# Kernel optimization log

Hardware: AMD Instinct MI355X
Metric: run time of the kernel (lower is better)

Reference implementation:

```python
import jax, jax.numpy as jnp
import numpy as np


def setup_inputs() -> dict:
    key = jax.random.key(0)
    k1, k2 = jax.random.split(key)
    N = 50000
    E = 800000
    out_features = 64
    edge = jax.random.randint(k1, (2, E), 0, N, dtype=jnp.int64)
    edge_w = jax.random.normal(k2, (E, out_features), dtype=jnp.float32)
    return {"edge": edge, "edge_w": edge_w, "N": N, "E": E, "out_features": out_features}


def reference(edge, edge_w, N, E, out_features):
    # sparse_coo_tensor(edge, edge_w, [N, N, F]) summed over dim=1 reduces to a
    # segment-sum of edge values over the row (source) index edge[0].
    # output[i, f] = sum_{e: edge[0,e]==i} edge_w[e, f]   -> [N, out_features]
    return jax.ops.segment_sum(edge_w, edge[0], num_segments=N)
```

## Files before the change

kernel.cpp:

```cpp
#include <hip/hip_runtime.h>


#define TILE 1024

__global__ __launch_bounds__(256) void hist_kernel(
    const int* __restrict__ edge0, int* __restrict__ counts, int E)
{
    int t = blockIdx.x * blockDim.x + threadIdx.x;
    int base = t * 4;
    if (base + 3 < E) {
        int4 r = ((const int4*)edge0)[t];
        atomicAdd(&counts[r.x], 1);
        atomicAdd(&counts[r.y], 1);
        atomicAdd(&counts[r.z], 1);
        atomicAdd(&counts[r.w], 1);
    } else {
        for (int i = base; i < E; ++i) atomicAdd(&counts[edge0[i]], 1);
    }
}

__global__ __launch_bounds__(256) void scan_partial(
    const int* __restrict__ counts, int* __restrict__ tileSum, int N)
{
    __shared__ int wsum[4];
    int t = threadIdx.x;
    int base = blockIdx.x * TILE + t * 4;
    int s = 0;
    #pragma unroll
    for (int k = 0; k < 4; ++k) {
        int i = base + k;
        if (i < N) s += counts[i];
    }
    for (int off = 1; off < 64; off <<= 1) s += __shfl_xor(s, off);
    if ((t & 63) == 0) wsum[t >> 6] = s;
    __syncthreads();
    if (t == 0) tileSum[blockIdx.x] = wsum[0] + wsum[1] + wsum[2] + wsum[3];
}

__global__ __launch_bounds__(64) void scan_tiles(
    const int* __restrict__ tileSum, int* __restrict__ tileOff, int numTiles,
    int* __restrict__ offsets, int N, int E)
{
    int t = threadIdx.x;
    int v0 = (t < numTiles) ? tileSum[t] : 0;
    int v = v0;
    for (int off = 1; off < 64; off <<= 1) {
        int u = __shfl_up(v, off);
        if (t >= off) v += u;
    }
    if (t < numTiles) tileOff[t] = v - v0;
    if (t == 0) offsets[N] = E;
}

__global__ __launch_bounds__(256) void scan_final(
    const int* __restrict__ counts, const int* __restrict__ tileOff,
    int* __restrict__ offsets, int N)
{
    __shared__ int wtot[4];
    int t = threadIdx.x;
    int lane = t & 63, wv = t >> 6;
    int base = blockIdx.x * TILE + t * 4;
    int c[4]; int s = 0;
    #pragma unroll
    for (int k = 0; k < 4; ++k) {
        int i = base + k;
        c[k] = (i < N) ? counts[i] : 0;
        s += c[k];
    }
    int inc = s;
    for (int off = 1; off < 64; off <<= 1) {
        int u = __shfl_up(inc, off);
        if (lane >= off) inc += u;
    }
    if (lane == 63) wtot[wv] = inc;
    __syncthreads();
    int wpre = 0;
    for (int w = 0; w < wv; ++w) wpre += wtot[w];
    int pre = tileOff[blockIdx.x] + wpre + (inc - s);
    #pragma unroll
    for (int k = 0; k < 4; ++k) {
        int i = base + k;
        if (i < N) offsets[i] = pre;
        pre += c[k];
    }
}

__global__ __launch_bounds__(256) void scatter_kernel(
    const int* __restrict__ edge0, int* __restrict__ cursor,
    int* __restrict__ ids, int E)
{
    int t = blockIdx.x * blockDim.x + threadIdx.x;
    int base = t * 4;
    if (base + 3 < E) {
        int4 r = ((const int4*)edge0)[t];
        ids[atomicAdd(&cursor[r.x], 1)] = base;
        ids[atomicAdd(&cursor[r.y], 1)] = base + 1;
        ids[atomicAdd(&cursor[r.z], 1)] = base + 2;
        ids[atomicAdd(&cursor[r.w], 1)] = base + 3;
    } else {
        for (int i = base; i < E; ++i) ids[atomicAdd(&cursor[edge0[i]], 1)] = i;
    }
}

__global__ __launch_bounds__(256) void reduce_kernel(
    const int* __restrict__ offsets, const int* __restrict__ ids,
    const float4* __restrict__ w4, float4* __restrict__ out4, int N)
{
    int row = blockIdx.x * 4 + (threadIdx.x >> 6);
    if (row >= N) return;
    int lane = threadIdx.x & 63;
    int sub = lane >> 3, g = lane & 7;
    int beg = offsets[row], end = offsets[row + 1];
    float4 a0 = make_float4(0.f, 0.f, 0.f, 0.f);
    float4 a1 = make_float4(0.f, 0.f, 0.f, 0.f);
    int j = beg + sub;
    for (; j + 8 < end; j += 16) {
        int e0 = ids[j], e1 = ids[j + 8];
        float4 w00 = w4[(size_t)e0 * 16 + g * 2];
        float4 w01 = w4[(size_t)e0 * 16 + g * 2 + 1];
        float4 w10 = w4[(size_t)e1 * 16 + g * 2];
        float4 w11 = w4[(size_t)e1 * 16 + g * 2 + 1];
        a0.x += w00.x + w10.x; a0.y += w00.y + w10.y;
        a0.z += w00.z + w10.z; a0.w += w00.w + w10.w;
        a1.x += w01.x + w11.x; a1.y += w01.y + w11.y;
        a1.z += w01.z + w11.z; a1.w += w01.w + w11.w;
    }
    if (j < end) {
        int e = ids[j];
        float4 w0 = w4[(size_t)e * 16 + g * 2];
        float4 w1 = w4[(size_t)e * 16 + g * 2 + 1];
        a0.x += w0.x; a0.y += w0.y; a0.z += w0.z; a0.w += w0.w;
        a1.x += w1.x; a1.y += w1.y; a1.z += w1.z; a1.w += w1.w;
    }
    #pragma unroll
    for (int m = 8; m < 64; m <<= 1) {
        a0.x += __shfl_xor(a0.x, m); a0.y += __shfl_xor(a0.y, m);
        a0.z += __shfl_xor(a0.z, m); a0.w += __shfl_xor(a0.w, m);
        a1.x += __shfl_xor(a1.x, m); a1.y += __shfl_xor(a1.y, m);
        a1.z += __shfl_xor(a1.z, m); a1.w += __shfl_xor(a1.w, m);
    }
    if (sub == 0) {
        out4[(size_t)row * 16 + g * 2]     = a0;
        out4[(size_t)row * 16 + g * 2 + 1] = a1;
    }
}

extern "C" void kernel_launch(void* const* d_in, const int* in_sizes, int n_in,
                              void* d_out, int out_size, void* d_ws, size_t ws_size,
                              hipStream_t stream) {
    const int*   edge   = (const int*)d_in[0];
    const float* edge_w = (const float*)d_in[1];
    int E = in_sizes[0] / 2;
    int N = out_size / 64;
    int numTiles = (N + TILE - 1) / TILE;

    int* counts  = (int*)d_ws;
    int* offsets = counts + N;
    int* cursor  = offsets + N + 1;
    int* ids     = cursor + N;
    int* tileSum = ids + E;
    int* tileOff = tileSum + 64;

    (void)hipMemsetAsync(counts, 0, (size_t)N * sizeof(int), stream);

    int blocksE = (E + 1023) / 1024;
    hist_kernel<<<blocksE, 256, 0, stream>>>(edge, counts, E);
    scan_partial<<<numTiles, 256, 0, stream>>>(counts, tileSum, N);
    scan_tiles<<<1, 64, 0, stream>>>(tileSum, tileOff, numTiles, offsets, N, E);
    scan_final<<<numTiles, 256, 0, stream>>>(counts, tileOff, offsets, N);
    (void)hipMemcpyAsync(cursor, offsets, (size_t)N * sizeof(int),
                         hipMemcpyDeviceToDevice, stream);
    scatter_kernel<<<blocksE, 256, 0, stream>>>(edge, cursor, ids, E);

    int blocksR = (N + 3) / 4;
    reduce_kernel<<<blocksR, 256, 0, stream>>>(offsets, ids, (const float4*)edge_w,
                                               (float4*)d_out, N);
}
```

Before: 385.6 us.

## Record per-edge rank in histogram to remove scatter atomics and cursor copy

The histogram kernel now stores the value returned by each atomicAdd as a per-edge rank. The scatter pass then computes positions as offsets plus rank, with no atomics and no cursor buffer, so the device-to-device memcpy goes away. The single-block tile scan is folded into scan_final, where each block recomputes the tile prefix redundantly, removing one launch. This adds an E-sized rank buffer that is written once and read once.

```diff
diff --git a/kernel.cpp b/kernel.cpp
--- a/kernel.cpp
+++ b/kernel.cpp
@@ -3,19 +3,22 @@
 
 #define TILE 1024
 
-__global__ __launch_bounds__(256) void hist_kernel(
-    const int* __restrict__ edge0, int* __restrict__ counts, int E)
+__global__ __launch_bounds__(256) void hist_rank_kernel(
+    const int* __restrict__ edge0, int* __restrict__ counts,
+    int* __restrict__ rank, int E)
 {
     int t = blockIdx.x * blockDim.x + threadIdx.x;
     int base = t * 4;
     if (base + 3 < E) {
         int4 r = ((const int4*)edge0)[t];
-        atomicAdd(&counts[r.x], 1);
-        atomicAdd(&counts[r.y], 1);
-        atomicAdd(&counts[r.z], 1);
-        atomicAdd(&counts[r.w], 1);
+        int4 k;
+        k.x = atomicAdd(&counts[r.x], 1);
+        k.y = atomicAdd(&counts[r.y], 1);
+        k.z = atomicAdd(&counts[r.z], 1);
+        k.w = atomicAdd(&counts[r.w], 1);
+        ((int4*)rank)[t] = k;
     } else {
-        for (int i = base; i < E; ++i) atomicAdd(&counts[edge0[i]], 1);
+        for (int i = base; i < E; ++i) rank[i] = atomicAdd(&counts[edge0[i]], 1);
     }
 }
 
@@ -37,28 +40,27 @@
     if (t == 0) tileSum[blockIdx.x] = wsum[0] + wsum[1] + wsum[2] + wsum[3];
 }
 
-__global__ __launch_bounds__(64) void scan_tiles(
-    const int* __restrict__ tileSum, int* __restrict__ tileOff, int numTiles,
-    int* __restrict__ offsets, int N, int E)
-{
-    int t = threadIdx.x;
-    int v0 = (t < numTiles) ? tileSum[t] : 0;
-    int v = v0;
-    for (int off = 1; off < 64; off <<= 1) {
-        int u = __shfl_up(v, off);
-        if (t >= off) v += u;
-    }
-    if (t < numTiles) tileOff[t] = v - v0;
-    if (t == 0) offsets[N] = E;
-}
-
 __global__ __launch_bounds__(256) void scan_final(
-    const int* __restrict__ counts, const int* __restrict__ tileOff,
-    int* __restrict__ offsets, int N)
+    const int* __restrict__ counts, const int* __restrict__ tileSum,
+    int* __restrict__ offsets, int N, int E, int numTiles)
 {
     __shared__ int wtot[4];
+    __shared__ int tilePre;
     int t = threadIdx.x;
     int lane = t & 63, wv = t >> 6;
+
+    if (t < 64) {
+        int v0 = (t < numTiles) ? tileSum[t] : 0;
+        int v = v0;
+        #pragma unroll
+        for (int off = 1; off < 64; off <<= 1) {
+            int u = __shfl_up(v, off);
+            if (t >= off) v += u;
+        }
+        if (t == blockIdx.x) tilePre = v - v0;
+    }
+    if (blockIdx.x == 0 && t == 0) offsets[N] = E;
+
     int base = blockIdx.x * TILE + t * 4;
     int c[4]; int s = 0;
     #pragma unroll
@@ -68,6 +70,7 @@
         s += c[k];
     }
     int inc = s;
+    #pragma unroll
     for (int off = 1; off < 64; off <<= 1) {
         int u = __shfl_up(inc, off);
         if (lane >= off) inc += u;
@@ -76,7 +79,7 @@
     __syncthreads();
     int wpre = 0;
     for (int w = 0; w < wv; ++w) wpre += wtot[w];
-    int pre = tileOff[blockIdx.x] + wpre + (inc - s);
+    int pre = tilePre + wpre + (inc - s);
     #pragma unroll
     for (int k = 0; k < 4; ++k) {
         int i = base + k;
@@ -86,19 +89,20 @@
 }
 
 __global__ __launch_bounds__(256) void scatter_kernel(
-    const int* __restrict__ edge0, int* __restrict__ cursor,
-    int* __restrict__ ids, int E)
+    const int* __restrict__ edge0, const int* __restrict__ rank,
+    const int* __restrict__ offsets, int* __restrict__ ids, int E)
 {
     int t = blockIdx.x * blockDim.x + threadIdx.x;
     int base = t * 4;
     if (base + 3 < E) {
         int4 r = ((const int4*)edge0)[t];
-        ids[atomicAdd(&cursor[r.x], 1)] = base;
-        ids[atomicAdd(&cursor[r.y], 1)] = base + 1;
-        ids[atomicAdd(&cursor[r.z], 1)] = base + 2;
-        ids[atomicAdd(&cursor[r.w], 1)] = base + 3;
+        int4 k = ((const int4*)rank)[t];
+        ids[offsets[r.x] + k.x] = base;
+        ids[offsets[r.y] + k.y] = base + 1;
+        ids[offsets[r.z] + k.z] = base + 2;
+        ids[offsets[r.w] + k.w] = base + 3;
     } else {
-        for (int i = base; i < E; ++i) ids[atomicAdd(&cursor[edge0[i]], 1)] = i;
+        for (int i = base; i < E; ++i) ids[offsets[edge0[i]] + rank[i]] = i;
     }
 }
 
@@ -156,21 +160,17 @@
 
     int* counts  = (int*)d_ws;
     int* offsets = counts + N;
-    int* cursor  = offsets + N + 1;
-    int* ids     = cursor + N;
+    int* rank    = offsets + N + 1;
+    int* ids     = rank + E;
     int* tileSum = ids + E;
-    int* tileOff = tileSum + 64;
 
     (void)hipMemsetAsync(counts, 0, (size_t)N * sizeof(int), stream);
 
     int blocksE = (E + 1023) / 1024;
-    hist_kernel<<<blocksE, 256, 0, stream>>>(edge, counts, E);
+    hist_rank_kernel<<<blocksE, 256, 0, stream>>>(edge, counts, rank, E);
     scan_partial<<<numTiles, 256, 0, stream>>>(counts, tileSum, N);
-    scan_tiles<<<1, 64, 0, stream>>>(tileSum, tileOff, numTiles, offsets, N, E);
-    scan_final<<<numTiles, 256, 0, stream>>>(counts, tileOff, offsets, N);
-    (void)hipMemcpyAsync(cursor, offsets, (size_t)N * sizeof(int),
-                         hipMemcpyDeviceToDevice, stream);
-    scatter_kernel<<<blocksE, 256, 0, stream>>>(edge, cursor, ids, E);
+    scan_final<<<numTiles, 256, 0, stream>>>(counts, tileSum, offsets, N, E, numTiles);
+    scatter_kernel<<<blocksE, 256, 0, stream>>>(edge, rank, offsets, ids, E);
 
     int blocksR = (N + 3) / 4;
     reduce_kernel<<<blocksR, 256, 0, stream>>>(offsets, ids, (const float4*)edge_w,
```

Result: faster. 351.4 us (-8.9%).
